# Kernel optimization log

Hardware: AMD Instinct MI355X
Metric: run time of the kernel (lower is better)

## Reference

```python
import jax, jax.numpy as jnp
import numpy as np

NUM_HEADS = 32
NUM_KV_HEADS = 8
HEAD_DIM = 128
ROPE_THETA = 10000.0
NEG_INF = -1e9


def _rope_cos_sin(position_ids, head_dim, dtype):
    # inv_freq: [head_dim/2]
    inv_freq = 1.0 / (ROPE_THETA ** (jnp.arange(0, head_dim, 2, dtype=jnp.float32) / head_dim))
    # freqs: [B, S, head_dim/2]
    freqs = position_ids.astype(jnp.float32)[..., None] * inv_freq[None, None, :]
    emb = jnp.concatenate([freqs, freqs], axis=-1)  # [B, S, head_dim]
    return jnp.cos(emb).astype(dtype), jnp.sin(emb).astype(dtype)


def _rotate_half(x):
    x1, x2 = jnp.split(x, 2, axis=-1)
    return jnp.concatenate([-x2, x1], axis=-1)


def setup_inputs() -> dict:
    key = jax.random.key(0)
    k1, k2, k3, k4, k5 = jax.random.split(key, 5)
    B, S, H = 2, 2048, 4096
    scale = 1.0 / np.sqrt(H)
    return {
        "hidden_states": jax.random.normal(k1, (B, S, H), jnp.float32),
        "position_ids": jnp.broadcast_to(jnp.arange(S, dtype=jnp.int32)[None, :], (B, S)),
        "Wq": jax.random.normal(k2, (H, H), jnp.float32) * scale,
        "Wk": jax.random.normal(k3, (NUM_KV_HEADS * HEAD_DIM, H), jnp.float32) * scale,
        "Wv": jax.random.normal(k4, (NUM_KV_HEADS * HEAD_DIM, H), jnp.float32) * scale,
        "Wo": jax.random.normal(k5, (H, H), jnp.float32) * scale,
    }


def reference(hidden_states, position_ids, Wq, Wk, Wv, Wo):
    B, S, H = hidden_states.shape
    dtype = hidden_states.dtype
    n_rep = NUM_HEADS // NUM_KV_HEADS

    # QKV projections (torch Linear: x @ W.T)
    q = (hidden_states @ Wq.T).reshape(B, S, NUM_HEADS, HEAD_DIM).transpose(0, 2, 1, 3)
    k = (hidden_states @ Wk.T).reshape(B, S, NUM_KV_HEADS, HEAD_DIM).transpose(0, 2, 1, 3)
    v = (hidden_states @ Wv.T).reshape(B, S, NUM_KV_HEADS, HEAD_DIM).transpose(0, 2, 1, 3)

    # RoPE (cos/sin broadcast over heads)
    cos, sin = _rope_cos_sin(position_ids, HEAD_DIM, dtype)
    cos, sin = cos[:, None, :, :], sin[:, None, :, :]  # [B,1,S,D]
    q = q * cos + _rotate_half(q) * sin
    k = k * cos + _rotate_half(k) * sin

    # repeat_kv (GQA): [B, KVH, S, D] -> [B, KVH*n_rep, S, D]
    k = jnp.repeat(k, n_rep, axis=1)
    v = jnp.repeat(v, n_rep, axis=1)

    # scaled dot-product attention with causal mask, softmax in fp32
    scores = jnp.einsum('bhqd,bhkd->bhqk', q, k) / np.sqrt(HEAD_DIM)
    causal = jnp.tril(jnp.ones((S, S), dtype=bool))
    scores = jnp.where(causal[None, None, :, :], scores, NEG_INF)
    probs = jax.nn.softmax(scores.astype(jnp.float32), axis=-1).astype(dtype)

    attn = jnp.einsum('bhqk,bhkd->bhqd', probs, v)
    attn = attn.transpose(0, 2, 1, 3).reshape(B, S, H)
    return attn @ Wo.T
```

## Files before the change

### kernel.cpp

```cpp
#include <hip/hip_runtime.h>

#define S_LEN 2048
#define BATCH 2
#define HID 4096
#define NH 32
#define NKV 8
#define DH 128
#define MROWS (BATCH*S_LEN)
#define QKV_N 6144

typedef unsigned short u16;
typedef unsigned int u32;
typedef __bf16 bf16x8 __attribute__((ext_vector_type(8)));
typedef float f32x4 __attribute__((ext_vector_type(4)));
typedef u16 u16x8 __attribute__((ext_vector_type(8)));

__device__ __forceinline__ u16 f2bf(float f) {
  union { float f; u32 u; } v; v.f = f;
  return (u16)((v.u + 0x8000u) >> 16);
}
__device__ __forceinline__ float bf2f(u16 h) {
  union { u32 u; float f; } v; v.u = ((u32)h) << 16;
  return v.f;
}
__device__ __forceinline__ u32 cvtpk(float a, float b) {
  u32 r;
  asm("v_cvt_pk_bf16_f32 %0, %1, %2" : "=v"(r) : "v"(a), "v"(b));
  return r;
}
__device__ __forceinline__ void async16(const void* g, void* l) {
  __builtin_amdgcn_global_load_lds(
      (const __attribute__((address_space(1))) u32*)g,
      (__attribute__((address_space(3))) u32*)l, 16, 0, 0);
}
__device__ __forceinline__ f32x4 mfma16(bf16x8 a, bf16x8 b, f32x4 c) {
  return __builtin_amdgcn_mfma_f32_16x16x32_bf16(a, b, c, 0, 0, 0);
}

#define BAR()    __builtin_amdgcn_s_barrier()
#define LGKM0()  asm volatile("s_waitcnt lgkmcnt(0)" ::: "memory")
#define PRIO(x)  __builtin_amdgcn_s_setprio(x)

__global__ __launch_bounds__(256) void cvt_f32_bf16(const float* __restrict__ in,
                                                    u16* __restrict__ out, int n) {
  int i0 = (blockIdx.x * 256 + threadIdx.x) * 8;
  if (i0 >= n) return;
  float4 a = *(const float4*)(in + i0);
  float4 b = *(const float4*)(in + i0 + 4);
  u16x8 r;
  r[0]=f2bf(a.x); r[1]=f2bf(a.y); r[2]=f2bf(a.z); r[3]=f2bf(a.w);
  r[4]=f2bf(b.x); r[5]=f2bf(b.y); r[6]=f2bf(b.z); r[7]=f2bf(b.w);
  *(u16x8*)(out + i0) = r;
}

template<int OUT_BF16>
__global__ __launch_bounds__(512, 2) void gemm256(
    const u16* __restrict__ A, const u16* __restrict__ B, void* __restrict__ Cout,
    int M, int N, int K, int XC, int SR, int SC) {
  __shared__ u16 As[2][2][64 * 128];
  __shared__ u16 Bs[2][2][64 * 128];
  const int NKT = K >> 6;
  int bid = (int)blockIdx.x;
  int xcd = bid & 7, l = bid >> 3;
  int tm = (xcd / XC) * SR + l / SC;
  int tn = (xcd % XC) * SC + l % SC;
  int m0 = tm << 8, n0 = tn << 8;
  int t = threadIdx.x;
  int w = t >> 6, lane = t & 63, lo = lane & 15, hi = lane >> 4;
  int wm = w >> 2, wn = w & 3;
  int rbb = (wn & 1) << 6;

  int srow = (w << 3) + (lane >> 3);
  int scol = (lane & 7) << 3;

  auto stageA = [&](int kt, int buf, int h) {
#pragma unroll
    for (int c2 = 0; c2 < 2; ++c2) {
      int row = (c2 << 6) + srow;
      int col = scol ^ ((row & 7) << 3);
      async16(A + (size_t)(m0 + (h << 7) + row) * K + (kt << 6) + col,
              (char*)&As[buf][h][0] + (c2 << 13) + (w << 10));
    }
  };
  auto stageB = [&](int kt, int buf, int h) {
#pragma unroll
    for (int c2 = 0; c2 < 2; ++c2) {
      int row = (c2 << 6) + srow;
      int col = scol ^ ((row & 7) << 3);
      async16(B + (size_t)(n0 + (h << 7) + row) * K + (kt << 6) + col,
              (char*)&Bs[buf][h][0] + (c2 << 13) + (w << 10));
    }
  };

  const f32x4 fz = {0.f, 0.f, 0.f, 0.f};
  f32x4 acc[8][4];
#pragma unroll
  for (int i = 0; i < 8; ++i)
#pragma unroll
    for (int j = 0; j < 4; ++j) acc[i][j] = fz;
  bf16x8 af[4][2], bf0[2][2], bf1[2][2];

  auto rdA = [&](int c, int half, bf16x8 (&dst)[4][2]) {
    const u16* Ab = &As[c][wm][0];
#pragma unroll
    for (int mf = 0; mf < 4; ++mf)
#pragma unroll
      for (int ks = 0; ks < 2; ++ks) {
        int ra = (half << 6) + (mf << 4) + lo;
        dst[mf][ks] = *(const bf16x8*)(Ab + (ra << 6) +
                      (((ks << 5) + (hi << 3)) ^ ((ra & 7) << 3)));
      }
  };
  auto rdB = [&](int c, int bfrag, bf16x8 (&dst)[2][2]) {
    const u16* Bb = &Bs[c][wn >> 1][0];
#pragma unroll
    for (int nf = 0; nf < 2; ++nf)
#pragma unroll
      for (int ks = 0; ks < 2; ++ks) {
        int rb = rbb + (bfrag << 5) + (nf << 4) + lo;
        dst[nf][ks] = *(const bf16x8*)(Bb + (rb << 6) +
                      (((ks << 5) + (hi << 3)) ^ ((rb & 7) << 3)));
      }
  };
  auto MM = [&](bf16x8 (&a)[4][2], bf16x8 (&b)[2][2], int mo, int no) {
#pragma unroll
    for (int mf = 0; mf < 4; ++mf)
#pragma unroll
      for (int nf = 0; nf < 2; ++nf)
#pragma unroll
        for (int ks = 0; ks < 2; ++ks)
          acc[mo + mf][no + nf] = mfma16(a[mf][ks], b[nf][ks], acc[mo + mf][no + nf]);
  };

#define VM4()    asm volatile("s_waitcnt vmcnt(4)" ::: "memory")
  stageA(0, 0, 0); stageA(0, 0, 1);
  stageB(0, 0, 0); stageB(0, 0, 1);
  stageB(1, 1, 0); stageB(1, 1, 1);
  VM4();
  BAR();

  const int NT = NKT >> 1;
  for (int it = 0; it < NT; ++it) {
    int e = it << 1, o = e + 1;
    int e2 = (e + 2 >= NKT) ? 0 : e + 2;
    int o2 = (o + 2 >= NKT) ? 1 : o + 2;

    rdA(0, 0, af); rdB(0, 0, bf0);
    stageA(o, 1, 0);
    BAR(); LGKM0(); PRIO(1);
    MM(af, bf0, 0, 0);
    PRIO(0); BAR();

    rdB(0, 1, bf1);
    stageA(o, 1, 1);
    BAR(); LGKM0(); PRIO(1);
    MM(af, bf1, 0, 2);
    PRIO(0); BAR();

    rdA(0, 1, af);
    stageB(e2, 0, 0);
    BAR(); LGKM0(); PRIO(1);
    MM(af, bf1, 4, 2);
    PRIO(0); BAR();

    stageB(e2, 0, 1);
    BAR(); PRIO(1);
    MM(af, bf0, 4, 0);
    PRIO(0); VM4(); BAR();

    rdA(1, 0, af); rdB(1, 0, bf0);
    stageA(e2, 0, 0);
    BAR(); LGKM0(); PRIO(1);
    MM(af, bf0, 0, 0);
    PRIO(0); BAR();

    rdB(1, 1, bf1);
    stageA(e2, 0, 1);
    BAR(); LGKM0(); PRIO(1);
    MM(af, bf1, 0, 2);
    PRIO(0); BAR();

    rdA(1, 1, af);
    stageB(o2, 1, 0);
    BAR(); LGKM0(); PRIO(1);
    MM(af, bf1, 4, 2);
    PRIO(0); BAR();

    stageB(o2, 1, 1);
    BAR(); PRIO(1);
    MM(af, bf0, 4, 0);
    PRIO(0); VM4(); BAR();
  }
#undef VM4

#pragma unroll
  for (int mf = 0; mf < 8; ++mf)
#pragma unroll
    for (int nf = 0; nf < 4; ++nf)
#pragma unroll
      for (int r = 0; r < 4; ++r) {
        int row = m0 + (wm << 7) + (mf << 4) + (hi << 2) + r;
        int col = n0 + (wn << 6) + (nf << 4) + lo;
        if (OUT_BF16) ((u16*)Cout)[(size_t)row * N + col] = f2bf(acc[mf][nf][r]);
        else          ((float*)Cout)[(size_t)row * N + col] = acc[mf][nf][r];
      }
}

__global__ __launch_bounds__(256) void rope_kernel(u16* __restrict__ X,
                                                   const int* __restrict__ pos,
                                                   int ncols, int pitch, float scale) {
  int idx = blockIdx.x * 256 + threadIdx.x;
  int groups = ncols >> 3;
  int m = idx / groups;
  int gi = idx - m * groups;
  if (m >= MROWS) return;
  int head = gi >> 4;
  int d0 = (gi & 15) << 2;
  float p = (float)pos[m];
  u16* base = X + (size_t)m * pitch + head * 128;
  u16 xa[4], xb[4], oa[4], ob[4];
  *(uint2*)xa = *(const uint2*)(base + d0);
  *(uint2*)xb = *(const uint2*)(base + d0 + 64);
#pragma unroll
  for (int i = 0; i < 4; ++i) {
    float j = (float)(d0 + i);
    float inv = __expf(j * -0.14391156516030342f);
    float fr = p * inv;
    float s, c;
    sincosf(fr, &s, &c);
    float x1 = bf2f(xa[i]), x2 = bf2f(xb[i]);
    oa[i] = f2bf((x1 * c - x2 * s) * scale);
    ob[i] = f2bf((x2 * c + x1 * s) * scale);
  }
  *(uint2*)(base + d0) = *(uint2*)oa;
  *(uint2*)(base + d0 + 64) = *(uint2*)ob;
}

__global__ __launch_bounds__(256) void transpose_v(const u16* __restrict__ V,
                                                   u16* __restrict__ Vt) {
  int bid = blockIdx.x;
  int s0 = (bid & 31) << 6;
  int bg = bid >> 5;
  int b = bg >> 3, g = bg & 7;
  __shared__ u16 tile[64][128];
  int t = threadIdx.x;
#pragma unroll
  for (int r = 0; r < 4; ++r) {
    int c = (r << 8) + t;
    int row = c >> 4, cc = c & 15;
    *(uint4*)&tile[row][cc * 8] =
        *(const uint4*)(V + (size_t)(b * S_LEN + s0 + row) * QKV_N + g * 128 + cc * 8);
  }
  __syncthreads();
#pragma unroll
  for (int r = 0; r < 4; ++r) {
    int c = (r << 8) + t;
    int d = c >> 3, cs = c & 7;
    u16 tmp[8];
#pragma unroll
    for (int i = 0; i < 8; ++i) tmp[i] = tile[cs * 8 + i][d];
    *(uint4*)(Vt + ((size_t)bg * 128 + d) * S_LEN + s0 + cs * 8) = *(uint4*)tmp;
  }
}

__global__ __launch_bounds__(256) void attn_kernel(
    const u16* __restrict__ Q, const u16* __restrict__ K,
    const u16* __restrict__ Vt, u16* __restrict__ O) {
  int bid = blockIdx.x;
  int qt = 31 - (bid >> 6);
  int bh = bid & 63;
  int b = bh >> 5, h = bh & 31;
  int g = h >> 2;
  __shared__ u16 Kl[2][64 * 128];
  __shared__ u16 Vl[2][128 * 64];
  __shared__ u16 Pl[4][16 * 72];
  int t = threadIdx.x, w = t >> 6, lane = t & 63, lo = lane & 15, hi = lane >> 4;

  bf16x8 qf[4];
  {
    const u16* qb = Q + (size_t)(b * S_LEN + (qt << 6) + (w << 4) + lo) * QKV_N + h * 128;
#pragma unroll
    for (int kk = 0; kk < 4; ++kk) qf[kk] = *(const bf16x8*)(qb + kk * 32 + hi * 8);
  }
  const f32x4 fz = {0.f, 0.f, 0.f, 0.f};
  f32x4 acc[8];
#pragma unroll
  for (int f = 0; f < 8; ++f) acc[f] = fz;
  float mrun = -1e30f, lrun = 0.f;

  const u16* Kbase = K + (size_t)(b * S_LEN) * QKV_N + g * 128;
  const u16* Vbase = Vt + (size_t)((b << 3) + g) * 128 * S_LEN;

  auto stageKV = [&](int tile, int buf) {
    int s0 = tile << 6;
#pragma unroll
    for (int r = 0; r < 4; ++r) {
      int c = (r << 8) + (w << 6) + lane;
      int row = c >> 4, cc = c & 15;
      int src = cc ^ (row & 7);
      async16(Kbase + (size_t)(s0 + row) * QKV_N + src * 8,
              (char*)&Kl[buf][0] + (r << 12) + (w << 10));
    }
#pragma unroll
    for (int r = 0; r < 4; ++r) {
      int c = (r << 8) + (w << 6) + lane;
      int row = c >> 3, cc = c & 7;
      int src = cc ^ (row & 7);
      async16(Vbase + (size_t)row * S_LEN + s0 + src * 8,
              (char*)&Vl[buf][0] + (r << 12) + (w << 10));
    }
  };

  int ntiles = qt + 1;
  stageKV(0, 0);
  __syncthreads();

  for (int tile = 0; tile < ntiles; ++tile) {
    int c = tile & 1;
    if (tile + 1 < ntiles) stageKV(tile + 1, c ^ 1);

    f32x4 sf[4];
#pragma unroll
    for (int j = 0; j < 4; ++j) {
      f32x4 sv = fz;
#pragma unroll
      for (int kk = 0; kk < 4; ++kk) {
        int row = (j << 4) + lo;
        int ch = ((kk << 2) + hi) ^ (row & 7);
        bf16x8 kf = *(const bf16x8*)(&Kl[c][0] + row * 128 + ch * 8);
        sv = __builtin_amdgcn_mfma_f32_16x16x32_bf16(kf, qf[kk], sv, 0, 0, 0);
      }
      sf[j] = sv;
    }
    if (tile == qt) {
      int q_rel = (w << 4) + lo;
#pragma unroll
      for (int j = 0; j < 4; ++j)
#pragma unroll
        for (int r = 0; r < 4; ++r)
          if (((j << 4) + (hi << 2) + r) > q_rel) sf[j][r] = -1e9f;
    }
    float pmax = sf[0][0];
#pragma unroll
    for (int j = 0; j < 4; ++j)
#pragma unroll
      for (int r = 0; r < 4; ++r) pmax = fmaxf(pmax, sf[j][r]);
    pmax = fmaxf(pmax, __shfl_xor(pmax, 16, 64));
    pmax = fmaxf(pmax, __shfl_xor(pmax, 32, 64));
    if (__any(pmax > mrun + 8.f)) {
      float mn = fmaxf(mrun, pmax);
      float fsc = __expf(mrun - mn);
      mrun = mn;
      lrun *= fsc;
#pragma unroll
      for (int f = 0; f < 8; ++f)
#pragma unroll
        for (int r = 0; r < 4; ++r) acc[f][r] *= fsc;
    }
    float psum = 0.f;
#pragma unroll
    for (int j = 0; j < 4; ++j)
#pragma unroll
      for (int r = 0; r < 4; ++r) {
        float p = __expf(sf[j][r] - mrun);
        sf[j][r] = p;
        psum += p;
      }
    psum += __shfl_xor(psum, 16, 64);
    psum += __shfl_xor(psum, 32, 64);
    lrun += psum;

#pragma unroll
    for (int j = 0; j < 4; ++j) {
      uint2 pk;
      pk.x = cvtpk(sf[j][0], sf[j][1]);
      pk.y = cvtpk(sf[j][2], sf[j][3]);
      *(uint2*)&Pl[w][lo * 72 + (j << 4) + (hi << 2)] = pk;
    }
#pragma unroll
    for (int kk = 0; kk < 2; ++kk) {
      bf16x8 pf = *(const bf16x8*)&Pl[w][lo * 72 + (kk << 5) + (hi << 3)];
#pragma unroll
      for (int f = 0; f < 8; ++f) {
        int vrow = (f << 4) + lo;
        int phys = ((kk << 2) + hi) ^ (vrow & 7);
        bf16x8 vf = *(const bf16x8*)(&Vl[c][0] + vrow * 64 + phys * 8);
        acc[f] = __builtin_amdgcn_mfma_f32_16x16x32_bf16(vf, pf, acc[f], 0, 0, 0);
      }
    }
    __syncthreads();
  }

  float rl = 1.0f / lrun;
#pragma unroll
  for (int half = 0; half < 2; ++half) {
#pragma unroll
    for (int f2 = 0; f2 < 4; ++f2) {
      int f = (half << 2) + f2;
      uint2 pk;
      pk.x = cvtpk(acc[f][0] * rl, acc[f][1] * rl);
      pk.y = cvtpk(acc[f][2] * rl, acc[f][3] * rl);
      *(uint2*)&Pl[w][lo * 72 + (f2 << 4) + (hi << 2)] = pk;
    }
#pragma unroll
    for (int it = 0; it < 2; ++it) {
      int rowq = (lane >> 3) + (it << 3);
      int c8 = lane & 7;
      uint4 val = *(const uint4*)&Pl[w][rowq * 72 + c8 * 8];
      *(uint4*)(O + (size_t)(b * S_LEN + (qt << 6) + (w << 4) + rowq) * 4096 +
                h * 128 + (half << 6) + c8 * 8) = val;
    }
  }
}

extern "C" void kernel_launch(void* const* d_in, const int* in_sizes, int n_in,
                              void* d_out, int out_size, void* d_ws, size_t ws_size,
                              hipStream_t stream) {
  const float* hidden = (const float*)d_in[0];
  const int* pos = (const int*)d_in[1];
  const float* Wq = (const float*)d_in[2];
  const float* Wk = (const float*)d_in[3];
  const float* Wv = (const float*)d_in[4];
  const float* Wo = (const float*)d_in[5];
  float* out = (float*)d_out;

  u16* hb   = (u16*)d_ws;
  u16* wqb  = hb   + 16777216;
  u16* wkb  = wqb  + 16777216;
  u16* wvb  = wkb  + 4194304;
  u16* wob  = wvb  + 4194304;
  u16* QKVb = wob  + 16777216;
  u16* Vtb  = QKVb + 25165824;
  u16* Ob   = Vtb  + 4194304;

  cvt_f32_bf16<<<8192, 256, 0, stream>>>(hidden, hb, 16777216);
  cvt_f32_bf16<<<8192, 256, 0, stream>>>(Wq, wqb, 16777216);
  cvt_f32_bf16<<<2048, 256, 0, stream>>>(Wk, wkb, 4194304);
  cvt_f32_bf16<<<2048, 256, 0, stream>>>(Wv, wvb, 4194304);
  cvt_f32_bf16<<<8192, 256, 0, stream>>>(Wo, wob, 16777216);

  gemm256<1><<<384, 512, 0, stream>>>(hb, wqb, QKVb, 4096, QKV_N, 4096, 4, 8, 6);

  rope_kernel<<<8192, 256, 0, stream>>>(QKVb, pos, 4096, QKV_N, 0.08838834764831845f);
  rope_kernel<<<2048, 256, 0, stream>>>(QKVb + 4096, pos, 1024, QKV_N, 1.0f);

  transpose_v<<<512, 256, 0, stream>>>(QKVb + 5120, Vtb);

  attn_kernel<<<2048, 256, 0, stream>>>(QKVb, QKVb + 4096, Vtb, Ob);

  gemm256<0><<<256, 512, 0, stream>>>(Ob, wob, out, 4096, 4096, 4096, 2, 4, 8);
}
```

Baseline: 541.7 us.

## Split tail tiles of QKV GEMM with split-K and a reduce kernel

Splits the 384-tile QKV projection GEMM into a 256-tile full-K launch plus a split-K launch that computes the remaining 128 tiles in two K halves into fp32 partial buffers. A new reduce kernel sums the halves and writes bf16 into the QKV buffer. The partial buffers reuse the Wo and attention-output workspace, so the Wo conversion is moved after the reduce. This aims to balance work across CUs at the cost of extra launches and fp32 partial traffic.

```diff
diff --git a/kernel.cpp b/kernel.cpp
--- a/kernel.cpp
+++ b/kernel.cpp
@@ -53,17 +53,28 @@
   *(u16x8*)(out + i0) = r;
 }
 
-template<int OUT_BF16>
+template<int MODE>
 __global__ __launch_bounds__(512, 2) void gemm256(
     const u16* __restrict__ A, const u16* __restrict__ B, void* __restrict__ Cout,
-    int M, int N, int K, int XC, int SR, int SC) {
+    int M, int N, int K, int XC, int SR, int SC,
+    int kSpan, int nkt, int tileBase, float* p0, float* p1) {
   __shared__ u16 As[2][2][64 * 128];
   __shared__ u16 Bs[2][2][64 * 128];
-  const int NKT = K >> 6;
+  const int NKT = nkt;
   int bid = (int)blockIdx.x;
-  int xcd = bid & 7, l = bid >> 3;
-  int tm = (xcd / XC) * SR + l / SC;
-  int tn = (xcd % XC) * SC + l % SC;
+  int tm, tn, half = 0, slot = 0;
+  if (MODE == 0) {
+    int xcd = bid & 7, l = bid >> 3;
+    tm = (xcd / XC) * SR + l / SC;
+    tn = (xcd % XC) * SC + l % SC;
+  } else {
+    int nTN = N >> 8;
+    int lin;
+    if (MODE == 2) { half = bid >> 7; slot = bid & 127; lin = tileBase + slot; }
+    else           { lin = tileBase + bid; }
+    tm = lin / nTN; tn = lin - tm * nTN;
+  }
+  const int koff = (MODE == 2) ? half * kSpan : 0;
   int m0 = tm << 8, n0 = tn << 8;
   int t = threadIdx.x;
   int w = t >> 6, lane = t & 63, lo = lane & 15, hi = lane >> 4;
@@ -78,7 +89,7 @@
     for (int c2 = 0; c2 < 2; ++c2) {
       int row = (c2 << 6) + srow;
       int col = scol ^ ((row & 7) << 3);
-      async16(A + (size_t)(m0 + (h << 7) + row) * K + (kt << 6) + col,
+      async16(A + (size_t)(m0 + (h << 7) + row) * K + (kt << 6) + koff + col,
               (char*)&As[buf][h][0] + (c2 << 13) + (w << 10));
     }
   };
@@ -87,7 +98,7 @@
     for (int c2 = 0; c2 < 2; ++c2) {
       int row = (c2 << 6) + srow;
       int col = scol ^ ((row & 7) << 3);
-      async16(B + (size_t)(n0 + (h << 7) + row) * K + (kt << 6) + col,
+      async16(B + (size_t)(n0 + (h << 7) + row) * K + (kt << 6) + koff + col,
               (char*)&Bs[buf][h][0] + (c2 << 13) + (w << 10));
     }
   };
@@ -100,13 +111,13 @@
     for (int j = 0; j < 4; ++j) acc[i][j] = fz;
   bf16x8 af[4][2], bf0[2][2], bf1[2][2];
 
-  auto rdA = [&](int c, int half, bf16x8 (&dst)[4][2]) {
+  auto rdA = [&](int c, int halfT, bf16x8 (&dst)[4][2]) {
     const u16* Ab = &As[c][wm][0];
 #pragma unroll
     for (int mf = 0; mf < 4; ++mf)
 #pragma unroll
       for (int ks = 0; ks < 2; ++ks) {
-        int ra = (half << 6) + (mf << 4) + lo;
+        int ra = (halfT << 6) + (mf << 4) + lo;
         dst[mf][ks] = *(const bf16x8*)(Ab + (ra << 6) +
                       (((ks << 5) + (hi << 3)) ^ ((ra & 7) << 3)));
       }
@@ -193,17 +204,43 @@
   }
 #undef VM4
 
+  float* dst = (MODE == 2) ? ((half ? p1 : p0) + (size_t)slot * 65536) : nullptr;
 #pragma unroll
   for (int mf = 0; mf < 8; ++mf)
 #pragma unroll
     for (int nf = 0; nf < 4; ++nf)
 #pragma unroll
       for (int r = 0; r < 4; ++r) {
-        int row = m0 + (wm << 7) + (mf << 4) + (hi << 2) + r;
-        int col = n0 + (wn << 6) + (nf << 4) + lo;
-        if (OUT_BF16) ((u16*)Cout)[(size_t)row * N + col] = f2bf(acc[mf][nf][r]);
-        else          ((float*)Cout)[(size_t)row * N + col] = acc[mf][nf][r];
-      }
+        int r_l = (wm << 7) + (mf << 4) + (hi << 2) + r;
+        int c_l = (wn << 6) + (nf << 4) + lo;
+        if (MODE == 2) {
+          dst[(size_t)r_l * 256 + c_l] = acc[mf][nf][r];
+        } else {
+          int row = m0 + r_l, col = n0 + c_l;
+          if (MODE == 1) ((u16*)Cout)[(size_t)row * N + col] = f2bf(acc[mf][nf][r]);
+          else           ((float*)Cout)[(size_t)row * N + col] = acc[mf][nf][r];
+        }
+      }
+}
+
+__global__ __launch_bounds__(256) void reduce_splitk(const float* __restrict__ p0,
+                                                     const float* __restrict__ p1,
+                                                     u16* __restrict__ C) {
+  int g = blockIdx.x * 256 + threadIdx.x;
+  int s = g >> 13;
+  int loc = g & 8191;
+  int r_l = loc >> 5, c8 = loc & 31;
+  int lin = 256 + s;
+  int tm = lin / 24, tn = lin - tm * 24;
+  size_t off = (size_t)s * 65536 + r_l * 256 + c8 * 8;
+  float4 x0 = *(const float4*)(p0 + off);
+  float4 x1 = *(const float4*)(p0 + off + 4);
+  float4 y0 = *(const float4*)(p1 + off);
+  float4 y1 = *(const float4*)(p1 + off + 4);
+  u16x8 r;
+  r[0]=f2bf(x0.x+y0.x); r[1]=f2bf(x0.y+y0.y); r[2]=f2bf(x0.z+y0.z); r[3]=f2bf(x0.w+y0.w);
+  r[4]=f2bf(x1.x+y1.x); r[5]=f2bf(x1.y+y1.y); r[6]=f2bf(x1.z+y1.z); r[7]=f2bf(x1.w+y1.w);
+  *(u16x8*)(C + (size_t)(tm * 256 + r_l) * QKV_N + tn * 256 + c8 * 8) = r;
 }
 
 __global__ __launch_bounds__(256) void rope_kernel(u16* __restrict__ X,
@@ -432,14 +469,21 @@
   u16* QKVb = wob  + 16777216;
   u16* Vtb  = QKVb + 25165824;
   u16* Ob   = Vtb  + 4194304;
+  float* part0 = (float*)wob;
+  float* part1 = (float*)Ob;
 
   cvt_f32_bf16<<<8192, 256, 0, stream>>>(hidden, hb, 16777216);
   cvt_f32_bf16<<<8192, 256, 0, stream>>>(Wq, wqb, 16777216);
   cvt_f32_bf16<<<2048, 256, 0, stream>>>(Wk, wkb, 4194304);
   cvt_f32_bf16<<<2048, 256, 0, stream>>>(Wv, wvb, 4194304);
+
+  gemm256<1><<<256, 512, 0, stream>>>(hb, wqb, QKVb, 4096, QKV_N, 4096,
+                                      0, 0, 0, 0, 64, 0, nullptr, nullptr);
+  gemm256<2><<<256, 512, 0, stream>>>(hb, wqb, QKVb, 4096, QKV_N, 4096,
+                                      0, 0, 0, 2048, 32, 256, part0, part1);
+  reduce_splitk<<<4096, 256, 0, stream>>>(part0, part1, QKVb);
+
   cvt_f32_bf16<<<8192, 256, 0, stream>>>(Wo, wob, 16777216);
-
-  gemm256<1><<<384, 512, 0, stream>>>(hb, wqb, QKVb, 4096, QKV_N, 4096, 4, 8, 6);
 
   rope_kernel<<<8192, 256, 0, stream>>>(QKVb, pos, 4096, QKV_N, 0.08838834764831845f);
   rope_kernel<<<2048, 256, 0, stream>>>(QKVb + 4096, pos, 1024, QKV_N, 1.0f);
@@ -448,5 +492,6 @@
 
   attn_kernel<<<2048, 256, 0, stream>>>(QKVb, QKVb + 4096, Vtb, Ob);
 
-  gemm256<0><<<256, 512, 0, stream>>>(Ob, wob, out, 4096, 4096, 4096, 2, 4, 8);
-}
+  gemm256<0><<<256, 512, 0, stream>>>(Ob, wob, out, 4096, 4096, 4096,
+                                      2, 4, 8, 0, 64, 0, nullptr, nullptr);
+}
```

Result: faster. 516.2 us (-4.7%).
